# Performance work log

Measured on AMD Instinct MI355X. Metric: run time of the kernel, lower is better.

## Reference

```python
import jax, jax.numpy as jnp
import numpy as np

B, L, H, NH = 8, 1024, 1024, 16
HD = H // NH  # head_dim = 64
SCALE = HD ** -0.5


def setup_inputs() -> dict:
    key = jax.random.key(0)
    kx, kqkv, kw, kb = jax.random.split(key, 4)
    x = jax.random.normal(kx, (B, L, H), dtype=jnp.float32)
    # nn.Linear(H, 3H, bias=False): weight [3H, H]
    w_qkv = jax.random.normal(kqkv, (3 * H, H), dtype=jnp.float32) * (H ** -0.5)
    # out_proj: nn.Linear(H, H) with bias
    w_out = jax.random.normal(kw, (H, H), dtype=jnp.float32) * (H ** -0.5)
    b_out = jax.random.normal(kb, (H,), dtype=jnp.float32) * 0.01
    return {"x": x, "w_qkv": w_qkv, "w_out": w_out, "b_out": b_out}


def reference(x, w_qkv, w_out, b_out):
    # qkv projection: [B, L, 3H]
    qkv = jnp.einsum('bld,ed->ble', x, w_qkv)
    # rearrange 'b l (qkv h d) -> qkv b h l d'
    qkv = qkv.reshape(B, L, 3, NH, HD)
    q = qkv[:, :, 0].transpose(0, 2, 1, 3)  # [B, NH, L, HD]
    k = qkv[:, :, 1].transpose(0, 2, 1, 3)
    v = qkv[:, :, 2].transpose(0, 2, 1, 3)
    att = jnp.einsum('bhxd,bhyd->bhxy', q, k) * SCALE
    att = jax.nn.softmax(att, axis=-1)
    o = jnp.einsum('bhxy,bhyd->bhxd', att, v)  # [B, NH, L, HD]
    o = o.transpose(0, 2, 1, 3).reshape(B, L, H)
    return jnp.einsum('bld,ed->ble', o, w_out) + b_out
```

## Files before the change

### kernel.cpp

```cpp
#include <hip/hip_runtime.h>


typedef short s16x8 __attribute__((ext_vector_type(8)));
typedef float f32x4 __attribute__((ext_vector_type(4)));
typedef unsigned int u32x2 __attribute__((ext_vector_type(2)));
typedef unsigned int u32x4 __attribute__((ext_vector_type(4)));

__device__ __forceinline__ unsigned short f2bf(float f) {
    union { float f; unsigned u; } c; c.f = f;
    return (unsigned short)((c.u + 0x7FFFu + ((c.u >> 16) & 1u)) >> 16);
}
__device__ __forceinline__ unsigned pack2bf(float a, float b) {
    union { float f; unsigned u; } ca, cb; ca.f = a; cb.f = b;
    return __builtin_amdgcn_perm(cb.u + 0x8000u, ca.u + 0x8000u, 0x07060302u);
}

#define GLOAD_LDS(g, l) __builtin_amdgcn_global_load_lds( \
    (const __attribute__((address_space(1))) void*)(g),   \
    (__attribute__((address_space(3))) void*)(l), 16, 0, 0)

__global__ __launch_bounds__(256) void cvt3(
    const float* __restrict__ s0, unsigned short* __restrict__ d0, int n0,
    const float* __restrict__ s1, unsigned short* __restrict__ d1, int n1,
    const float* __restrict__ s2, unsigned short* __restrict__ d2, int n2)
{
    long i = ((long)blockIdx.x * 256 + threadIdx.x) * 8;
    const float* s; unsigned short* d; long off;
    if (i < n0)                  { s = s0; d = d0; off = i; }
    else if (i < (long)n0 + n1)  { s = s1; d = d1; off = i - n0; }
    else                         { s = s2; d = d2; off = i - n0 - n1; }
    f32x4 a = *(const f32x4*)(s + off);
    f32x4 b = *(const f32x4*)(s + off + 4);
    u32x4 r;
    r[0] = pack2bf(a[0], a[1]); r[1] = pack2bf(a[2], a[3]);
    r[2] = pack2bf(b[0], b[1]); r[3] = pack2bf(b[2], b[3]);
    *(u32x4*)(d + off) = r;
}

template<int EPI>
__global__ __launch_bounds__(256) void gemm16(
    const unsigned short* __restrict__ A, const unsigned short* __restrict__ Bm,
    unsigned short* __restrict__ Cq, unsigned short* __restrict__ Cv,
    float* __restrict__ Cf, const float* __restrict__ bias,
    int N, int K)
{
    __shared__ unsigned short As[128 * 64];
    __shared__ unsigned short Bs[128 * 64];
    const int tid = threadIdx.x, lane = tid & 63, wave = tid >> 6;
    const int quad = lane >> 4, l16 = lane & 15;
    const int wm = (wave >> 1) * 64, wn = (wave & 1) * 64;
    const int m0 = blockIdx.y * 128, n0 = blockIdx.x * 128;

    const int prow = tid >> 3;
    const int qch  = (tid & 7) ^ (prow & 7);
    const unsigned short* gA[4];
    const unsigned short* gB[4];
    #pragma unroll
    for (int c = 0; c < 4; ++c) {
        gA[c] = A + (size_t)(m0 + c * 32 + prow) * K + qch * 8;
        gB[c] = Bm + (size_t)(n0 + c * 32 + prow) * K + qch * 8;
    }
    const int sw = l16 & 7;

    f32x4 acc[4][4] = {};
    for (int k0 = 0; k0 < K; k0 += 64) {
        __syncthreads();
        #pragma unroll
        for (int c = 0; c < 4; ++c) {
            GLOAD_LDS(gA[c], As + (c * 256 + tid) * 8);
            GLOAD_LDS(gB[c], Bs + (c * 256 + tid) * 8);
            gA[c] += 64; gB[c] += 64;
        }
        __syncthreads();
        #pragma unroll
        for (int s = 0; s < 2; ++s) {
            s16x8 af[4], bf[4];
            const int pc = ((s * 4 + quad) ^ sw) * 8;
            #pragma unroll
            for (int i = 0; i < 4; ++i)
                af[i] = *(const s16x8*)(As + (wm + i * 16 + l16) * 64 + pc);
            #pragma unroll
            for (int j = 0; j < 4; ++j)
                bf[j] = *(const s16x8*)(Bs + (wn + j * 16 + l16) * 64 + pc);
            #pragma unroll
            for (int i = 0; i < 4; ++i)
                #pragma unroll
                for (int j = 0; j < 4; ++j)
                    acc[i][j] = __builtin_amdgcn_mfma_f32_16x16x32_bf16(af[i], bf[j], acc[i][j], 0, 0, 0);
        }
    }

    if (EPI == 1) {
        #pragma unroll
        for (int j = 0; j < 4; ++j) {
            int col = n0 + wn + j * 16 + l16;
            float bv = bias[col];
            #pragma unroll
            for (int i = 0; i < 4; ++i)
                #pragma unroll
                for (int r = 0; r < 4; ++r)
                    Cf[(size_t)(m0 + wm + i * 16 + quad * 4 + r) * N + col] = acc[i][j][r] + bv;
        }
    } else if (n0 < 2048) {
        #pragma unroll
        for (int j = 0; j < 4; ++j) {
            int col = n0 + wn + j * 16 + l16;
            #pragma unroll
            for (int i = 0; i < 4; ++i)
                #pragma unroll
                for (int r = 0; r < 4; ++r)
                    Cq[(size_t)(m0 + wm + i * 16 + quad * 4 + r) * 2048 + col] = f2bf(acc[i][j][r]);
        }
    } else {
        #pragma unroll
        for (int j = 0; j < 4; ++j) {
            int dcol = n0 + wn + j * 16 + l16 - 2048;
            int hh = dcol >> 6, dd = dcol & 63;
            #pragma unroll
            for (int i = 0; i < 4; ++i) {
                int row = m0 + wm + i * 16 + quad * 4;
                int bb = row >> 10, l = row & 1023;
                u32x2 pw;
                pw[0] = pack2bf(acc[i][j][0], acc[i][j][1]);
                pw[1] = pack2bf(acc[i][j][2], acc[i][j][3]);
                *(u32x2*)(Cv + (size_t)((bb * 16 + hh) * 64 + dd) * 1024 + l) = pw;
            }
        }
    }
}

__global__ __launch_bounds__(256) void attn(
    const unsigned short* __restrict__ qk, const unsigned short* __restrict__ Vt,
    unsigned short* __restrict__ O)
{
    __shared__ unsigned short Ks[64 * 64];
    __shared__ unsigned short Vs[64 * 64];
    __shared__ unsigned short Ps[4][16 * 72];

    const int bh = blockIdx.x, b = bh >> 4, hh = bh & 15;
    const int q0 = blockIdx.y * 128;
    const int tid = threadIdx.x, lane = tid & 63, wave = tid >> 6;
    const int quad = lane >> 4, l16 = lane & 15;

    s16x8 qf[2][2];
    #pragma unroll
    for (int h = 0; h < 2; ++h) {
        const unsigned short* qrow =
            qk + (size_t)(b * 1024 + q0 + h * 64 + wave * 16 + l16) * 2048 + hh * 64;
        qf[h][0] = *(const s16x8*)(qrow + quad * 8);
        qf[h][1] = *(const s16x8*)(qrow + 32 + quad * 8);
    }

    const int rl = lane >> 3;
    const int qc = (lane & 7) ^ rl;
    const int g0 = wave * 2, g1 = g0 + 1;
    const unsigned short* srcK0 = qk + (size_t)(b * 1024 + g0 * 8 + rl) * 2048 + 1024 + hh * 64 + qc * 8;
    const unsigned short* srcK1 = qk + (size_t)(b * 1024 + g1 * 8 + rl) * 2048 + 1024 + hh * 64 + qc * 8;
    const unsigned short* srcV0 = Vt + (size_t)(bh * 64 + g0 * 8 + rl) * 1024 + qc * 8;
    const unsigned short* srcV1 = Vt + (size_t)(bh * 64 + g1 * 8 + rl) * 1024 + qc * 8;
    unsigned short* dK0 = Ks + g0 * 512 + lane * 8;
    unsigned short* dK1 = Ks + g1 * 512 + lane * 8;
    unsigned short* dV0 = Vs + g0 * 512 + lane * 8;
    unsigned short* dV1 = Vs + g1 * 512 + lane * 8;

    const int sw = l16 & 7;

    f32x4 Oacc[2][4] = {};
    float lsum[2] = {0.0f, 0.0f};

    for (int kv = 0; kv < 1024; kv += 64) {
        __syncthreads();
        GLOAD_LDS(srcK0, dK0);
        GLOAD_LDS(srcK1, dK1);
        GLOAD_LDS(srcV0, dV0);
        GLOAD_LDS(srcV1, dV1);
        srcK0 += (size_t)64 * 2048; srcK1 += (size_t)64 * 2048;
        srcV0 += 64; srcV1 += 64;
        __syncthreads();

        #pragma unroll
        for (int h = 0; h < 2; ++h) {
            unsigned short* Pw = &Ps[wave][0];
            f32x4 Sacc[4] = {};
            #pragma unroll
            for (int j = 0; j < 4; ++j) {
                #pragma unroll
                for (int s = 0; s < 2; ++s) {
                    s16x8 kf = *(const s16x8*)(Ks + (j * 16 + l16) * 64 + ((s * 4 + quad) ^ sw) * 8);
                    Sacc[j] = __builtin_amdgcn_mfma_f32_16x16x32_bf16(kf, qf[h][s], Sacc[j], 0, 0, 0);
                }
            }
            #pragma unroll
            for (int j = 0; j < 4; ++j) {
                float p0 = __expf(Sacc[j][0] * 0.125f);
                float p1 = __expf(Sacc[j][1] * 0.125f);
                float p2 = __expf(Sacc[j][2] * 0.125f);
                float p3 = __expf(Sacc[j][3] * 0.125f);
                lsum[h] += (p0 + p1) + (p2 + p3);
                u32x2 pw;
                pw[0] = pack2bf(p0, p1);
                pw[1] = pack2bf(p2, p3);
                *(u32x2*)(Pw + l16 * 72 + j * 16 + quad * 4) = pw;
            }
            asm volatile("s_waitcnt lgkmcnt(0)" ::: "memory");
            #pragma unroll
            for (int s = 0; s < 2; ++s) {
                s16x8 pf = *(const s16x8*)(Pw + l16 * 72 + s * 32 + quad * 8);
                #pragma unroll
                for (int j = 0; j < 4; ++j) {
                    s16x8 vf = *(const s16x8*)(Vs + (j * 16 + l16) * 64 + ((s * 4 + quad) ^ sw) * 8);
                    Oacc[h][j] = __builtin_amdgcn_mfma_f32_16x16x32_bf16(pf, vf, Oacc[h][j], 0, 0, 0);
                }
            }
        }
    }

    #pragma unroll
    for (int h = 0; h < 2; ++h) {
        float ls = lsum[h];
        ls += __shfl_xor(ls, 16, 64);
        ls += __shfl_xor(ls, 32, 64);
        float rinv[4];
        #pragma unroll
        for (int r = 0; r < 4; ++r)
            rinv[r] = 1.0f / __shfl(ls, quad * 4 + r, 64);
        #pragma unroll
        for (int j = 0; j < 4; ++j)
            #pragma unroll
            for (int r = 0; r < 4; ++r) {
                int row = q0 + h * 64 + wave * 16 + quad * 4 + r;
                int col = hh * 64 + j * 16 + l16;
                O[(size_t)(b * 1024 + row) * 1024 + col] = f2bf(Oacc[h][j][r] * rinv[r]);
            }
    }
}

extern "C" void kernel_launch(void* const* d_in, const int* in_sizes, int n_in,
                              void* d_out, int out_size, void* d_ws, size_t ws_size,
                              hipStream_t stream) {
    const float* x     = (const float*)d_in[0];
    const float* w_qkv = (const float*)d_in[1];
    const float* w_out = (const float*)d_in[2];
    const float* b_out = (const float*)d_in[3];
    float* out = (float*)d_out;

    const int nx = 8192 * 1024, nwq = 3072 * 1024, nwo = 1024 * 1024;
    unsigned short* xb  = (unsigned short*)d_ws;
    unsigned short* wqb = xb + nx;
    unsigned short* wob = wqb + nwq;
    unsigned short* qkb = wob + nwo;
    unsigned short* Vt  = qkb + (size_t)8192 * 2048;
    unsigned short* Ob  = xb;

    dim3 blk(256);
    cvt3<<<6144, blk, 0, stream>>>(x, xb, nx, w_qkv, wqb, nwq, w_out, wob, nwo);
    gemm16<0><<<dim3(24, 64), blk, 0, stream>>>(xb, wqb, qkb, Vt, nullptr, nullptr, 3072, 1024);
    attn<<<dim3(128, 8), blk, 0, stream>>>(qkb, Vt, Ob);
    gemm16<1><<<dim3(8, 64), blk, 0, stream>>>(Ob, wob, nullptr, nullptr, out, b_out, 1024, 1024);
}
```

Measured before the change: 248.1 us.

## Double-buffer K/V tiles in attention to overlap global loads with MFMA

The attention kernel now keeps two LDS buffers for the K and V tiles. It prefetches the next 64-key tile with global_load_lds while computing on the current one, and drops to one barrier per iteration instead of two. The P scratch buffer is also split per half so the two q-halves do not reuse the same LDS region. The aim is to hide global load latency behind the QK^T and PV matrix work, at the cost of roughly twice the LDS use per block, which may lower occupancy.

```diff
diff --git a/kernel.cpp b/kernel.cpp
--- a/kernel.cpp
+++ b/kernel.cpp
@@ -133,9 +133,9 @@
     const unsigned short* __restrict__ qk, const unsigned short* __restrict__ Vt,
     unsigned short* __restrict__ O)
 {
-    __shared__ unsigned short Ks[64 * 64];
-    __shared__ unsigned short Vs[64 * 64];
-    __shared__ unsigned short Ps[4][16 * 72];
+    __shared__ unsigned short Ks[2][64 * 64];
+    __shared__ unsigned short Vs[2][64 * 64];
+    __shared__ unsigned short Ps[4][2][16 * 72];
 
     const int bh = blockIdx.x, b = bh >> 4, hh = bh & 15;
     const int q0 = blockIdx.y * 128;
@@ -158,35 +158,43 @@
     const unsigned short* srcK1 = qk + (size_t)(b * 1024 + g1 * 8 + rl) * 2048 + 1024 + hh * 64 + qc * 8;
     const unsigned short* srcV0 = Vt + (size_t)(bh * 64 + g0 * 8 + rl) * 1024 + qc * 8;
     const unsigned short* srcV1 = Vt + (size_t)(bh * 64 + g1 * 8 + rl) * 1024 + qc * 8;
-    unsigned short* dK0 = Ks + g0 * 512 + lane * 8;
-    unsigned short* dK1 = Ks + g1 * 512 + lane * 8;
-    unsigned short* dV0 = Vs + g0 * 512 + lane * 8;
-    unsigned short* dV1 = Vs + g1 * 512 + lane * 8;
+    const int oK0 = g0 * 512 + lane * 8, oK1 = g1 * 512 + lane * 8;
 
     const int sw = l16 & 7;
 
     f32x4 Oacc[2][4] = {};
     float lsum[2] = {0.0f, 0.0f};
 
-    for (int kv = 0; kv < 1024; kv += 64) {
+    GLOAD_LDS(srcK0, &Ks[0][0] + oK0);
+    GLOAD_LDS(srcK1, &Ks[0][0] + oK1);
+    GLOAD_LDS(srcV0, &Vs[0][0] + oK0);
+    GLOAD_LDS(srcV1, &Vs[0][0] + oK1);
+    srcK0 += (size_t)64 * 2048; srcK1 += (size_t)64 * 2048;
+    srcV0 += 64; srcV1 += 64;
+
+    for (int t = 0; t < 16; ++t) {
         __syncthreads();
-        GLOAD_LDS(srcK0, dK0);
-        GLOAD_LDS(srcK1, dK1);
-        GLOAD_LDS(srcV0, dV0);
-        GLOAD_LDS(srcV1, dV1);
-        srcK0 += (size_t)64 * 2048; srcK1 += (size_t)64 * 2048;
-        srcV0 += 64; srcV1 += 64;
-        __syncthreads();
+        const int cur = t & 1, nxt = cur ^ 1;
+        if (t < 15) {
+            GLOAD_LDS(srcK0, &Ks[nxt][0] + oK0);
+            GLOAD_LDS(srcK1, &Ks[nxt][0] + oK1);
+            GLOAD_LDS(srcV0, &Vs[nxt][0] + oK0);
+            GLOAD_LDS(srcV1, &Vs[nxt][0] + oK1);
+            srcK0 += (size_t)64 * 2048; srcK1 += (size_t)64 * 2048;
+            srcV0 += 64; srcV1 += 64;
+        }
+        const unsigned short* Kc = &Ks[cur][0];
+        const unsigned short* Vc = &Vs[cur][0];
 
         #pragma unroll
         for (int h = 0; h < 2; ++h) {
-            unsigned short* Pw = &Ps[wave][0];
+            unsigned short* Pw = &Ps[wave][h][0];
             f32x4 Sacc[4] = {};
             #pragma unroll
             for (int j = 0; j < 4; ++j) {
                 #pragma unroll
                 for (int s = 0; s < 2; ++s) {
-                    s16x8 kf = *(const s16x8*)(Ks + (j * 16 + l16) * 64 + ((s * 4 + quad) ^ sw) * 8);
+                    s16x8 kf = *(const s16x8*)(Kc + (j * 16 + l16) * 64 + ((s * 4 + quad) ^ sw) * 8);
                     Sacc[j] = __builtin_amdgcn_mfma_f32_16x16x32_bf16(kf, qf[h][s], Sacc[j], 0, 0, 0);
                 }
             }
@@ -208,7 +216,7 @@
                 s16x8 pf = *(const s16x8*)(Pw + l16 * 72 + s * 32 + quad * 8);
                 #pragma unroll
                 for (int j = 0; j < 4; ++j) {
-                    s16x8 vf = *(const s16x8*)(Vs + (j * 16 + l16) * 64 + ((s * 4 + quad) ^ sw) * 8);
+                    s16x8 vf = *(const s16x8*)(Vc + (j * 16 + l16) * 64 + ((s * 4 + quad) ^ sw) * 8);
                     Oacc[h][j] = __builtin_amdgcn_mfma_f32_16x16x32_bf16(pf, vf, Oacc[h][j], 0, 0, 0);
                 }
             }
```

New measurement: 257.5 us. 3.8% more time.
